# Kernel tuning notes

Hardware: AMD Instinct MI355X
Metric: run time of the kernel (lower is better)

Reference implementation:

```python
import jax, jax.numpy as jnp
import numpy as np


def setup_inputs() -> dict:
    key = jax.random.key(0)
    kx, kw = jax.random.split(key)
    x = jax.random.normal(kx, (32, 64, 112, 112), dtype=jnp.float32)
    weights = jax.random.normal(kw, (128, 64, 3, 3), dtype=jnp.float32)
    return {"x": x, "weights": weights}


def reference(x, weights):
    # The torch module's triple loop computes a standard VALID conv2d,
    # stride 1, no padding, weights shared across spatial locations.
    # x: [B, Cin, H, W]; weights: [Cout, Cin, k, k] -> out: [B, Cout, H-k+1, W-k+1]
    out = jax.lax.conv_general_dilated(
        x, weights,
        window_strides=(1, 1),
        padding="VALID",
        dimension_numbers=("NCHW", "OIHW", "NCHW"),
    )
    return out
```

## Files before the change

### kernel.cpp

```cpp
#include <hip/hip_runtime.h>


typedef short bf16x8 __attribute__((ext_vector_type(8)));
typedef float f32x4 __attribute__((ext_vector_type(4)));

__device__ __forceinline__ unsigned short f2bf(float f) {
    unsigned int u = __builtin_bit_cast(unsigned int, f);
    unsigned int r = u + 0x7fffu + ((u >> 16) & 1u);
    return (unsigned short)(r >> 16);
}
__device__ __forceinline__ unsigned int pack2(float lo, float hi) {
    return (unsigned)f2bf(lo) | ((unsigned)f2bf(hi) << 16);
}

__global__ void wperm_kernel(const float* __restrict__ W, unsigned short* __restrict__ wp) {
    int t = blockIdx.x * 256 + threadIdx.x;
    if (t < 73728) {
        int e    = t & 7;
        int l15  = (t >> 3) & 15;
        int quad = (t >> 7) & 3;
        int cs   = (t >> 9) & 1;
        int cog  = (t >> 10) & 7;
        int r    = t >> 13;
        int ci = cs * 32 + quad * 8 + e;
        int co = cog * 16 + l15;
        wp[t] = f2bf(W[(co * 64 + ci) * 9 + r]);
    }
}

__global__ __launch_bounds__(512, 4) void conv_mfma(const float* __restrict__ x,
                                                    const unsigned short* __restrict__ wp,
                                                    float* __restrict__ out) {
    __shared__ alignas(16) unsigned short xwin[324 * 72];

    const int tid  = threadIdx.x;
    const int lane = tid & 63;
    const int wv   = tid >> 6;
    const int wvoh = wv & 3;
    const int wvco = wv >> 1 & 0;
    const int quad = lane >> 4;
    const int l15  = lane & 15;

    const int wco  = wv >> 2;
    const int woh  = wv & 3;
    (void)wvoh; (void)wvco;

    const int blk  = blockIdx.x;
    const int xcd  = blk & 7;
    const int slot = blk >> 3;
    const int b    = xcd + 8 * (slot / 49);
    const int tile = slot % 49;
    const int oh0  = (tile / 7) * 16;
    const int ow0  = (tile % 7) * 16;

    const float* xb = x + b * 802816;

    for (int t = tid; t < 2304; t += 512) {
        const int cgl = t & 7;
        const int hwl = (t >> 3) & 7;
        const int cgh = (t >> 6) & 3;
        const int hwh = t >> 8;
        const int cg  = cgh * 8 + cgl;
        const int hw  = hwh * 8 + hwl;
        const int hh  = hw >> 2;
        const int wc  = hw & 3;
        const int h   = min(oh0 + hh, 111);
        const float* p0 = xb + (2 * cg) * 12544 + h * 112 + ow0 + wc * 4;
        const f32x4 a = *reinterpret_cast<const f32x4*>(p0);
        const f32x4 c = *reinterpret_cast<const f32x4*>(p0 + 12544);
        unsigned int* dst = reinterpret_cast<unsigned int*>(
            &xwin[(hh * 18 + wc * 4) * 72 + 2 * cg]);
        dst[0]   = pack2(a[0], c[0]);
        dst[36]  = pack2(a[1], c[1]);
        dst[72]  = pack2(a[2], c[2]);
        dst[108] = pack2(a[3], c[3]);
    }
    for (int u = tid; u < 576; u += 512) {
        const int cg  = u & 31;
        const int hh  = u >> 5;
        const int h   = min(oh0 + hh, 111);
        const int w16 = min(ow0 + 16, 111);
        const int w17 = min(ow0 + 17, 111);
        const float* p0 = xb + (2 * cg) * 12544 + h * 112;
        unsigned int* dst = reinterpret_cast<unsigned int*>(
            &xwin[(hh * 18 + 16) * 72 + 2 * cg]);
        dst[0]  = pack2(p0[w16], p0[12544 + w16]);
        dst[36] = pack2(p0[w17], p0[12544 + w17]);
    }

    f32x4 acc[4][4];
    const f32x4 zero = {0.0f, 0.0f, 0.0f, 0.0f};
    #pragma unroll
    for (int mt = 0; mt < 4; mt++)
        #pragma unroll
        for (int nt = 0; nt < 4; nt++) acc[mt][nt] = zero;

    __syncthreads();

    const bf16x8* wq = reinterpret_cast<const bf16x8*>(wp) + lane;
    const int cogb = wco * 4;

    #pragma unroll
    for (int r = 0; r < 9; r++) {
        const int kh = r / 3;
        const int kw = r % 3;
        #pragma unroll
        for (int cs = 0; cs < 2; cs++) {
            const int ko = cs * 32 + quad * 8;
            bf16x8 af[4];
            #pragma unroll
            for (int mt = 0; mt < 4; mt++)
                af[mt] = wq[((r * 8 + cogb + mt) * 2 + cs) * 64];
            bf16x8 bfrag[4];
            #pragma unroll
            for (int nt = 0; nt < 4; nt++)
                bfrag[nt] = *reinterpret_cast<const bf16x8*>(
                    &xwin[((woh * 4 + nt + kh) * 18 + (l15 + kw)) * 72 + ko]);
            __builtin_amdgcn_s_setprio(1);
            #pragma unroll
            for (int mt = 0; mt < 4; mt++)
                #pragma unroll
                for (int nt = 0; nt < 4; nt++)
                    acc[mt][nt] = __builtin_amdgcn_mfma_f32_16x16x32_bf16(
                        af[mt], bfrag[nt], acc[mt][nt], 0, 0, 0);
            __builtin_amdgcn_s_setprio(0);
        }
    }

    const int owc = ow0 + l15;
    if (owc < 110) {
        float* ob = out + b * 1548800 + wco * 64 * 12100;
        #pragma unroll
        for (int mt = 0; mt < 4; mt++) {
            #pragma unroll
            for (int nt = 0; nt < 4; nt++) {
                const int oh = oh0 + woh * 4 + nt;
                if (oh < 110) {
                    #pragma unroll
                    for (int reg = 0; reg < 4; reg++) {
                        const int co = mt * 16 + quad * 4 + reg;
                        ob[(co * 110 + oh) * 110 + owc] = acc[mt][nt][reg];
                    }
                }
            }
        }
    }
}

extern "C" void kernel_launch(void* const* d_in, const int* in_sizes, int n_in,
                              void* d_out, int out_size, void* d_ws, size_t ws_size,
                              hipStream_t stream) {
    const float* x = (const float*)d_in[0];
    const float* W = (const float*)d_in[1];
    float* out = (float*)d_out;
    unsigned short* wp = (unsigned short*)d_ws;

    wperm_kernel<<<288, 256, 0, stream>>>(W, wp);
    conv_mfma<<<32 * 49, 512, 0, stream>>>(x, wp, out);
}
```

Before: 353.4 us.

## Make conv kernel persistent with double-buffered LDS prefetch of next tile

Launches one block per CU that loops over spatial tiles, prefetching the next tile's input into registers while computing the current tile and writing the previous tile's output. The LDS window is double-buffered so the staging write happens after compute, with one barrier per tile. This aims to hide global load latency and launch overhead, but doubles LDS usage, lowers occupancy to a single block per CU, and introduces 7-vs-6 tile imbalance across blocks.

```diff
diff --git a/kernel.cpp b/kernel.cpp
--- a/kernel.cpp
+++ b/kernel.cpp
@@ -28,123 +28,189 @@
     }
 }
 
-__global__ __launch_bounds__(512, 4) void conv_mfma(const float* __restrict__ x,
+#define XWIN_SH 23328
+
+__global__ __launch_bounds__(512, 2) void conv_mfma(const float* __restrict__ x,
                                                     const unsigned short* __restrict__ wp,
                                                     float* __restrict__ out) {
-    __shared__ alignas(16) unsigned short xwin[324 * 72];
+    __shared__ alignas(16) unsigned short xwin[2 * XWIN_SH];
 
     const int tid  = threadIdx.x;
     const int lane = tid & 63;
     const int wv   = tid >> 6;
-    const int wvoh = wv & 3;
-    const int wvco = wv >> 1 & 0;
     const int quad = lane >> 4;
     const int l15  = lane & 15;
-
     const int wco  = wv >> 2;
     const int woh  = wv & 3;
-    (void)wvoh; (void)wvco;
-
-    const int blk  = blockIdx.x;
-    const int xcd  = blk & 7;
-    const int slot = blk >> 3;
-    const int b    = xcd + 8 * (slot / 49);
-    const int tile = slot % 49;
-    const int oh0  = (tile / 7) * 16;
-    const int ow0  = (tile % 7) * 16;
-
-    const float* xb = x + b * 802816;
-
-    for (int t = tid; t < 2304; t += 512) {
-        const int cgl = t & 7;
-        const int hwl = (t >> 3) & 7;
-        const int cgh = (t >> 6) & 3;
-        const int hwh = t >> 8;
-        const int cg  = cgh * 8 + cgl;
-        const int hw  = hwh * 8 + hwl;
-        const int hh  = hw >> 2;
-        const int wc  = hw & 3;
-        const int h   = min(oh0 + hh, 111);
-        const float* p0 = xb + (2 * cg) * 12544 + h * 112 + ow0 + wc * 4;
-        const f32x4 a = *reinterpret_cast<const f32x4*>(p0);
-        const f32x4 c = *reinterpret_cast<const f32x4*>(p0 + 12544);
-        unsigned int* dst = reinterpret_cast<unsigned int*>(
-            &xwin[(hh * 18 + wc * 4) * 72 + 2 * cg]);
-        dst[0]   = pack2(a[0], c[0]);
-        dst[36]  = pack2(a[1], c[1]);
-        dst[72]  = pack2(a[2], c[2]);
-        dst[108] = pack2(a[3], c[3]);
-    }
-    for (int u = tid; u < 576; u += 512) {
-        const int cg  = u & 31;
-        const int hh  = u >> 5;
-        const int h   = min(oh0 + hh, 111);
-        const int w16 = min(ow0 + 16, 111);
-        const int w17 = min(ow0 + 17, 111);
-        const float* p0 = xb + (2 * cg) * 12544 + h * 112;
-        unsigned int* dst = reinterpret_cast<unsigned int*>(
-            &xwin[(hh * 18 + 16) * 72 + 2 * cg]);
-        dst[0]  = pack2(p0[w16], p0[12544 + w16]);
-        dst[36] = pack2(p0[w17], p0[12544 + w17]);
-    }
+
+    const int blk    = blockIdx.x;
+    const int xcd    = blk & 7;
+    const int slot   = blk >> 3;
+    const int ntiles = (slot < 4) ? 7 : 6;
+
+    f32x4 sa[5], sc[5];
+    float hx[8];
+
+    auto stage_load = [&](int b, int oh0, int ow0) {
+        const float* xb = x + b * 802816;
+        #pragma unroll
+        for (int s = 0; s < 5; s++) {
+            const int t = tid + s * 512;
+            if (s < 4 || tid < 256) {
+                const int cg = (((t >> 6) & 3) << 3) | (t & 7);
+                const int hw = ((t >> 8) << 3) | ((t >> 3) & 7);
+                const int hh = hw >> 2;
+                const int wc = hw & 3;
+                const int h  = min(oh0 + hh, 111);
+                const float* p0 = xb + 2 * cg * 12544 + h * 112 + ow0 + wc * 4;
+                sa[s] = *reinterpret_cast<const f32x4*>(p0);
+                sc[s] = *reinterpret_cast<const f32x4*>(p0 + 12544);
+            }
+        }
+        #pragma unroll
+        for (int s = 0; s < 2; s++) {
+            const int u = tid + s * 512;
+            if (s == 0 || tid < 64) {
+                const int cg  = u & 31;
+                const int hh  = u >> 5;
+                const int h   = min(oh0 + hh, 111);
+                const int w16 = min(ow0 + 16, 111);
+                const int w17 = min(ow0 + 17, 111);
+                const float* p0 = xb + 2 * cg * 12544 + h * 112;
+                hx[s * 4 + 0] = p0[w16];
+                hx[s * 4 + 1] = p0[12544 + w16];
+                hx[s * 4 + 2] = p0[w17];
+                hx[s * 4 + 3] = p0[12544 + w17];
+            }
+        }
+    };
+
+    auto stage_write = [&](int buf) {
+        unsigned short* xw = xwin + buf * XWIN_SH;
+        #pragma unroll
+        for (int s = 0; s < 5; s++) {
+            const int t = tid + s * 512;
+            if (s < 4 || tid < 256) {
+                const int cg = (((t >> 6) & 3) << 3) | (t & 7);
+                const int hw = ((t >> 8) << 3) | ((t >> 3) & 7);
+                const int hh = hw >> 2;
+                const int wc = hw & 3;
+                unsigned int* dst = reinterpret_cast<unsigned int*>(
+                    &xw[(hh * 18 + wc * 4) * 72 + 2 * cg]);
+                dst[0]   = pack2(sa[s][0], sc[s][0]);
+                dst[36]  = pack2(sa[s][1], sc[s][1]);
+                dst[72]  = pack2(sa[s][2], sc[s][2]);
+                dst[108] = pack2(sa[s][3], sc[s][3]);
+            }
+        }
+        #pragma unroll
+        for (int s = 0; s < 2; s++) {
+            const int u = tid + s * 512;
+            if (s == 0 || tid < 64) {
+                const int cg = u & 31;
+                const int hh = u >> 5;
+                unsigned int* dst = reinterpret_cast<unsigned int*>(
+                    &xw[(hh * 18 + 16) * 72 + 2 * cg]);
+                dst[0]  = pack2(hx[s * 4 + 0], hx[s * 4 + 1]);
+                dst[36] = pack2(hx[s * 4 + 2], hx[s * 4 + 3]);
+            }
+        }
+    };
 
     f32x4 acc[4][4];
     const f32x4 zero = {0.0f, 0.0f, 0.0f, 0.0f};
-    #pragma unroll
-    for (int mt = 0; mt < 4; mt++)
-        #pragma unroll
-        for (int nt = 0; nt < 4; nt++) acc[mt][nt] = zero;
-
-    __syncthreads();
+
+    auto epilogue = [&](int b, int eoh0, int eow0) {
+        const int owc = eow0 + l15;
+        if (owc < 110) {
+            float* ob = out + b * 1548800 + wco * 64 * 12100;
+            #pragma unroll
+            for (int mt = 0; mt < 4; mt++) {
+                #pragma unroll
+                for (int nt = 0; nt < 4; nt++) {
+                    const int oh = eoh0 + woh * 4 + nt;
+                    if (oh < 110) {
+                        #pragma unroll
+                        for (int reg = 0; reg < 4; reg++) {
+                            const int co = mt * 16 + quad * 4 + reg;
+                            ob[(co * 110 + oh) * 110 + owc] = acc[mt][nt][reg];
+                        }
+                    }
+                }
+            }
+        }
+    };
 
     const bf16x8* wq = reinterpret_cast<const bf16x8*>(wp) + lane;
     const int cogb = wco * 4;
 
-    #pragma unroll
-    for (int r = 0; r < 9; r++) {
-        const int kh = r / 3;
-        const int kw = r % 3;
-        #pragma unroll
-        for (int cs = 0; cs < 2; cs++) {
-            const int ko = cs * 32 + quad * 8;
-            bf16x8 af[4];
+    {
+        const int t0 = slot;
+        const int b0 = xcd + 8 * (t0 / 49);
+        const int tl = t0 % 49;
+        stage_load(b0, (tl / 7) * 16, (tl % 7) * 16);
+        stage_write(0);
+    }
+    __syncthreads();
+
+    int cur = 0;
+    int pb = 0, poh = 0, pow_ = 0;
+
+    for (int j = 0; j < ntiles; j++) {
+        const int ti  = slot + 32 * j;
+        const int cb  = xcd + 8 * (ti / 49);
+        const int ct  = ti % 49;
+        const int coh = (ct / 7) * 16;
+        const int cow = (ct % 7) * 16;
+
+        const int ni = ti + 32;
+        if (ni < 196) {
+            const int nb  = xcd + 8 * (ni / 49);
+            const int ntl = ni % 49;
+            stage_load(nb, (ntl / 7) * 16, (ntl % 7) * 16);
+        }
+        if (j > 0) epilogue(pb, poh, pow_);
+
+        #pragma unroll
+        for (int mt = 0; mt < 4; mt++)
             #pragma unroll
-            for (int mt = 0; mt < 4; mt++)
-                af[mt] = wq[((r * 8 + cogb + mt) * 2 + cs) * 64];
-            bf16x8 bfrag[4];
+            for (int nt = 0; nt < 4; nt++) acc[mt][nt] = zero;
+
+        const unsigned short* xw = xwin + cur * XWIN_SH;
+        #pragma unroll
+        for (int r = 0; r < 9; r++) {
+            const int kh = r / 3;
+            const int kw = r % 3;
             #pragma unroll
-            for (int nt = 0; nt < 4; nt++)
-                bfrag[nt] = *reinterpret_cast<const bf16x8*>(
-                    &xwin[((woh * 4 + nt + kh) * 18 + (l15 + kw)) * 72 + ko]);
-            __builtin_amdgcn_s_setprio(1);
-            #pragma unroll
-            for (int mt = 0; mt < 4; mt++)
+            for (int cs = 0; cs < 2; cs++) {
+                const int ko = cs * 32 + quad * 8;
+                bf16x8 af[4];
+                #pragma unroll
+                for (int mt = 0; mt < 4; mt++)
+                    af[mt] = wq[((r * 8 + cogb + mt) * 2 + cs) * 64];
+                bf16x8 bfrag[4];
                 #pragma unroll
                 for (int nt = 0; nt < 4; nt++)
-                    acc[mt][nt] = __builtin_amdgcn_mfma_f32_16x16x32_bf16(
-                        af[mt], bfrag[nt], acc[mt][nt], 0, 0, 0);
-            __builtin_amdgcn_s_setprio(0);
-        }
+                    bfrag[nt] = *reinterpret_cast<const bf16x8*>(
+                        &xw[((woh * 4 + nt + kh) * 18 + (l15 + kw)) * 72 + ko]);
+                __builtin_amdgcn_s_setprio(1);
+                #pragma unroll
+                for (int mt = 0; mt < 4; mt++)
+                    #pragma unroll
+                    for (int nt = 0; nt < 4; nt++)
+                        acc[mt][nt] = __builtin_amdgcn_mfma_f32_16x16x32_bf16(
+                            af[mt], bfrag[nt], acc[mt][nt], 0, 0, 0);
+                __builtin_amdgcn_s_setprio(0);
+            }
+        }
+
+        if (ni < 196) stage_write(cur ^ 1);
+        __syncthreads();
+        pb = cb; poh = coh; pow_ = cow;
+        cur ^= 1;
     }
-
-    const int owc = ow0 + l15;
-    if (owc < 110) {
-        float* ob = out + b * 1548800 + wco * 64 * 12100;
-        #pragma unroll
-        for (int mt = 0; mt < 4; mt++) {
-            #pragma unroll
-            for (int nt = 0; nt < 4; nt++) {
-                const int oh = oh0 + woh * 4 + nt;
-                if (oh < 110) {
-                    #pragma unroll
-                    for (int reg = 0; reg < 4; reg++) {
-                        const int co = mt * 16 + quad * 4 + reg;
-                        ob[(co * 110 + oh) * 110 + owc] = acc[mt][nt][reg];
-                    }
-                }
-            }
-        }
-    }
+    epilogue(pb, poh, pow_);
+
 }
 
 extern "C" void kernel_launch(void* const* d_in, const int* in_sizes, int n_in,
@@ -156,5 +222,5 @@
     unsigned short* wp = (unsigned short*)d_ws;
 
     wperm_kernel<<<288, 256, 0, stream>>>(W, wp);
-    conv_mfma<<<32 * 49, 512, 0, stream>>>(x, wp, out);
-}
+    conv_mfma<<<256, 512, 0, stream>>>(x, wp, out);
+}
```

New measurement: 564.3 us. 59.7% more time.

## Pre-convert input to swizzled NHWC bf16 and run persistent double-buffered conv

Applied to the files above, without the earlier changes.

Adds a pre-pass kernel that converts the fp32 NCHW input into an XOR-swizzled channel-last bf16 copy in workspace. A persistent conv kernel (256 blocks, each looping over about 6-7 tiles) then stages tiles with direct global-to-LDS loads into a double buffer, so the next tile loads while the current one runs its MFMAs. The epilogue store of the previous tile is also overlapped. The trade-off is an extra full pass over the input and a large workspace requirement, with the old kernel kept as a fallback when workspace is too small.

```diff
diff --git a/kernel.cpp b/kernel.cpp
--- a/kernel.cpp
+++ b/kernel.cpp
@@ -1,4 +1,5 @@
 #include <hip/hip_runtime.h>
+#include <stdint.h>
 
 
 typedef short bf16x8 __attribute__((ext_vector_type(8)));
@@ -28,22 +29,179 @@
     }
 }
 
-__global__ __launch_bounds__(512, 4) void conv_mfma(const float* __restrict__ x,
-                                                    const unsigned short* __restrict__ wp,
-                                                    float* __restrict__ out) {
-    __shared__ alignas(16) unsigned short xwin[324 * 72];
+__global__ __launch_bounds__(256) void xconv_kernel(const float* __restrict__ x,
+                                                    unsigned short* __restrict__ xswz) {
+    __shared__ unsigned int row32[112 * 33];
+    const int bh = blockIdx.x;
+    const int b  = bh / 112;
+    const int h  = bh - b * 112;
+    const float* xb = x + (size_t)b * 802816 + h * 112;
+    for (int t = threadIdx.x; t < 3584; t += 256) {
+        const int cg = t / 112;
+        const int w  = t - cg * 112;
+        const float lo = xb[(2 * cg) * 12544 + w];
+        const float hi = xb[(2 * cg) * 12544 + 12544 + w];
+        row32[w * 33 + cg] = pack2(lo, hi);
+    }
+    __syncthreads();
+    unsigned short* ob = xswz + (size_t)bh * 7168;
+    for (int t = threadIdx.x; t < 896; t += 256) {
+        const int wl  = t >> 3;
+        const int c   = t & 7;
+        const int cg0 = (c ^ (wl & 7)) * 4;
+        uint4 v;
+        v.x = row32[wl * 33 + cg0 + 0];
+        v.y = row32[wl * 33 + cg0 + 1];
+        v.z = row32[wl * 33 + cg0 + 2];
+        v.w = row32[wl * 33 + cg0 + 3];
+        *reinterpret_cast<uint4*>(ob + t * 8) = v;
+    }
+}
+
+#define XW_SH   20992
+#define NCHUNK  2592
+
+__global__ __launch_bounds__(512, 2) void conv_mfma_dl(const unsigned short* __restrict__ xswz,
+                                                       const unsigned short* __restrict__ wp,
+                                                       float* __restrict__ out) {
+    __shared__ alignas(16) unsigned short xwin[2 * XW_SH];
 
     const int tid  = threadIdx.x;
     const int lane = tid & 63;
     const int wv   = tid >> 6;
-    const int wvoh = wv & 3;
-    const int wvco = wv >> 1 & 0;
     const int quad = lane >> 4;
     const int l15  = lane & 15;
-
     const int wco  = wv >> 2;
     const int woh  = wv & 3;
-    (void)wvoh; (void)wvco;
+
+    const int blk    = blockIdx.x;
+    const int xcd    = blk & 7;
+    const int slot   = blk >> 3;
+    const int ntiles = (slot < 4) ? 7 : 6;
+
+    auto stage = [&](int ti, int buf) {
+        const int b   = xcd + 8 * (ti / 49);
+        const int tl  = ti % 49;
+        const int oh0 = (tl / 7) * 16;
+        const int ow0 = (tl % 7) * 16;
+        const unsigned short* xbase = xswz + (size_t)b * 802816;
+        #pragma unroll
+        for (int it = 0; it < 6; ++it) {
+            const int cb = it * 512 + wv * 64;
+            const int ch = cb + lane;
+            if (ch < NCHUNK) {
+                const int pxc = ch >> 3;
+                const int c   = ch & 7;
+                const int hh  = pxc / 18;
+                const int col = pxc - hh * 18;
+                const int h   = min(oh0 + hh, 111);
+                const int w   = min(ow0 + col, 111);
+                __builtin_amdgcn_global_load_lds(
+                    (const __attribute__((address_space(1))) unsigned int*)
+                        (xbase + ((h * 112 + w) << 6) + c * 8),
+                    (__attribute__((address_space(3))) unsigned int*)
+                        (&xwin[buf * XW_SH + cb * 8]),
+                    16, 0, 0);
+            }
+        }
+    };
+
+    f32x4 acc[4][4];
+    const f32x4 zero = {0.0f, 0.0f, 0.0f, 0.0f};
+
+    auto epilogue = [&](int ti) {
+        const int b   = xcd + 8 * (ti / 49);
+        const int tl  = ti % 49;
+        const int oh0 = (tl / 7) * 16;
+        const int ow0 = (tl % 7) * 16;
+        const int owc = ow0 + l15;
+        if (owc < 110) {
+            float* ob = out + b * 1548800 + wco * 64 * 12100;
+            #pragma unroll
+            for (int mt = 0; mt < 4; mt++) {
+                #pragma unroll
+                for (int nt = 0; nt < 4; nt++) {
+                    const int oh = oh0 + woh * 4 + nt;
+                    if (oh < 110) {
+                        #pragma unroll
+                        for (int reg = 0; reg < 4; reg++) {
+                            const int co = mt * 16 + quad * 4 + reg;
+                            ob[(co * 110 + oh) * 110 + owc] = acc[mt][nt][reg];
+                        }
+                    }
+                }
+            }
+        }
+    };
+
+    const bf16x8* wq = reinterpret_cast<const bf16x8*>(wp) + lane;
+    const int cogb = wco * 4;
+
+    stage(slot, 0);
+    __syncthreads();
+
+    int cur = 0;
+    int pti = -1;
+
+    for (int j = 0; j < ntiles; j++) {
+        const int ti = slot + 32 * j;
+        const int ni = ti + 32;
+        if (ni < 196) stage(ni, cur ^ 1);
+        if (pti >= 0) epilogue(pti);
+
+        #pragma unroll
+        for (int mt = 0; mt < 4; mt++)
+            #pragma unroll
+            for (int nt = 0; nt < 4; nt++) acc[mt][nt] = zero;
+
+        const unsigned short* xw = xwin + cur * XW_SH;
+        #pragma unroll
+        for (int r = 0; r < 9; r++) {
+            const int kh = r / 3;
+            const int kw = r % 3;
+            const int col = l15 + kw;
+            #pragma unroll
+            for (int cs = 0; cs < 2; cs++) {
+                bf16x8 af[4];
+                #pragma unroll
+                for (int mt = 0; mt < 4; mt++)
+                    af[mt] = wq[((r * 8 + cogb + mt) * 2 + cs) * 64];
+                const int sl = ((cs * 4 + quad) ^ (col & 7)) * 8;
+                bf16x8 bfrag[4];
+                #pragma unroll
+                for (int nt = 0; nt < 4; nt++)
+                    bfrag[nt] = *reinterpret_cast<const bf16x8*>(
+                        &xw[((woh * 4 + nt + kh) * 18 + col) * 64 + sl]);
+                __builtin_amdgcn_s_setprio(1);
+                #pragma unroll
+                for (int mt = 0; mt < 4; mt++)
+                    #pragma unroll
+                    for (int nt = 0; nt < 4; nt++)
+                        acc[mt][nt] = __builtin_amdgcn_mfma_f32_16x16x32_bf16(
+                            af[mt], bfrag[nt], acc[mt][nt], 0, 0, 0);
+                __builtin_amdgcn_s_setprio(0);
+            }
+        }
+
+        __syncthreads();
+        pti = ti;
+        cur ^= 1;
+    }
+    epilogue(pti);
+}
+
+__global__ __launch_bounds__(512, 4) void conv_mfma_r4(const float* __restrict__ x,
+                                                       const unsigned short* __restrict__ wp,
+                                                       float* __restrict__ out) {
+    __shared__ alignas(16) unsigned short xwin[324 * 72];
+
+    const int tid  = threadIdx.x;
+    const int lane = tid & 63;
+    const int wv   = tid >> 6;
+    const int quad = lane >> 4;
+    const int l15  = lane & 15;
+    const int wco  = wv >> 2;
+    const int woh  = wv & 3;
 
     const int blk  = blockIdx.x;
     const int xcd  = blk & 7;
@@ -56,16 +214,12 @@
     const float* xb = x + b * 802816;
 
     for (int t = tid; t < 2304; t += 512) {
-        const int cgl = t & 7;
-        const int hwl = (t >> 3) & 7;
-        const int cgh = (t >> 6) & 3;
-        const int hwh = t >> 8;
-        const int cg  = cgh * 8 + cgl;
-        const int hw  = hwh * 8 + hwl;
-        const int hh  = hw >> 2;
-        const int wc  = hw & 3;
-        const int h   = min(oh0 + hh, 111);
-        const float* p0 = xb + (2 * cg) * 12544 + h * 112 + ow0 + wc * 4;
+        const int cg = (((t >> 6) & 3) << 3) | (t & 7);
+        const int hw = ((t >> 8) << 3) | ((t >> 3) & 7);
+        const int hh = hw >> 2;
+        const int wc = hw & 3;
+        const int h  = min(oh0 + hh, 111);
+        const float* p0 = xb + 2 * cg * 12544 + h * 112 + ow0 + wc * 4;
         const f32x4 a = *reinterpret_cast<const f32x4*>(p0);
         const f32x4 c = *reinterpret_cast<const f32x4*>(p0 + 12544);
         unsigned int* dst = reinterpret_cast<unsigned int*>(
@@ -81,7 +235,7 @@
         const int h   = min(oh0 + hh, 111);
         const int w16 = min(ow0 + 16, 111);
         const int w17 = min(ow0 + 17, 111);
-        const float* p0 = xb + (2 * cg) * 12544 + h * 112;
+        const float* p0 = xb + 2 * cg * 12544 + h * 112;
         unsigned int* dst = reinterpret_cast<unsigned int*>(
             &xwin[(hh * 18 + 16) * 72 + 2 * cg]);
         dst[0]  = pack2(p0[w16], p0[12544 + w16]);
@@ -156,5 +310,14 @@
     unsigned short* wp = (unsigned short*)d_ws;
 
     wperm_kernel<<<288, 256, 0, stream>>>(W, wp);
-    conv_mfma<<<32 * 49, 512, 0, stream>>>(x, wp, out);
-}
+
+    const size_t XOFF = 147456;
+    const size_t XB   = (size_t)32 * 112 * 112 * 64 * 2;
+    if (ws_size >= XOFF + XB) {
+        unsigned short* xswz = (unsigned short*)((char*)d_ws + XOFF);
+        xconv_kernel<<<32 * 112, 256, 0, stream>>>(x, xswz);
+        conv_mfma_dl<<<256, 512, 0, stream>>>(xswz, wp, out);
+    } else {
+        conv_mfma_r4<<<1568, 512, 0, stream>>>(x, wp, out);
+    }
+}
```

After: 512.2 us. 44.9% more time.
